# Performance work log

Measured on AMD Instinct MI355X. Metric: run time of the kernel, lower is better.

## Reference

```python
import jax, jax.numpy as jnp
import numpy as np
from jax import lax

# Module hyperparameters (from init_kwargs)
H, W, T = 80, 96, 112   # full-resolution feature volume size
C = 16                  # in_channel
K = 3                   # kernel_size (box filter)
D = 3                   # correlation window count per axis
SF = 2                  # correlation stride (sf)
CC = 2 * C + K ** 3     # conv1 in/out channels = 59


def _resize_axis_linear_ac(x, axis, out_size):
    """1D linear resize along `axis` with align_corners=True semantics."""
    in_size = x.shape[axis]
    pos = jnp.arange(out_size, dtype=x.dtype) * ((in_size - 1) / (out_size - 1))
    i0 = jnp.clip(jnp.floor(pos).astype(jnp.int32), 0, in_size - 2)
    w1 = pos - i0.astype(x.dtype)
    shp = [1] * x.ndim
    shp[axis] = out_size
    w1 = w1.reshape(shp)
    x0 = jnp.take(x, i0, axis=axis)
    x1 = jnp.take(x, i0 + 1, axis=axis)
    return x0 * (1.0 - w1) + x1 * w1


def upsample_trilinear_ac(x, factor=2):
    # matches nn.Upsample(scale_factor=2, mode='trilinear', align_corners=True)
    for axis in (2, 3, 4):
        x = _resize_axis_linear_ac(x, axis, x.shape[axis] * factor)
    return x


def _grid_sample_3d_one(src, coords):
    """src [C,H,W,T], coords [3,H,W,T] in voxel units.
    Trilinear sampling, zeros padding, align_corners=True (matches grid_sample)."""
    Hs, Ws, Ts = src.shape[1], src.shape[2], src.shape[3]
    cx, cy, cz = coords[0], coords[1], coords[2]
    x0 = jnp.floor(cx); y0 = jnp.floor(cy); z0 = jnp.floor(cz)
    fx = cx - x0; fy = cy - y0; fz = cz - z0
    x0i = x0.astype(jnp.int32); y0i = y0.astype(jnp.int32); z0i = z0.astype(jnp.int32)
    out = jnp.zeros_like(src)
    for dx in (0, 1):
        for dy in (0, 1):
            for dz in (0, 1):
                ix = x0i + dx; iy = y0i + dy; iz = z0i + dz
                valid = (ix >= 0) & (ix < Hs) & (iy >= 0) & (iy < Ws) & (iz >= 0) & (iz < Ts)
                v = src[:, jnp.clip(ix, 0, Hs - 1), jnp.clip(iy, 0, Ws - 1), jnp.clip(iz, 0, Ts - 1)]
                w = (fx if dx else 1.0 - fx) * (fy if dy else 1.0 - fy) * (fz if dz else 1.0 - fz)
                out = out + jnp.where(valid, w, 0.0)[None] * v
    return out


def spatial_transform(src, flow):
    # src [B,C,H,W,T], flow [B,3,H,W,T] (voxel displacement)
    grid = jnp.stack(jnp.meshgrid(jnp.arange(H), jnp.arange(W), jnp.arange(T), indexing='ij')).astype(src.dtype)
    coords = grid[None] + flow  # [B,3,H,W,T]
    return jax.vmap(_grid_sample_3d_one)(src, coords)


def _box3(x, pad):
    """Depthwise 3x3x3 ones-kernel conv with zero padding `pad` (separable box sum)."""
    x = jnp.pad(x, ((0, 0), (0, 0), (pad, pad), (pad, pad), (pad, pad)))
    for axis in (2, 3, 4):
        n = x.shape[axis]
        x = (lax.slice_in_dim(x, 0, n - 2, axis=axis)
             + lax.slice_in_dim(x, 1, n - 1, axis=axis)
             + lax.slice_in_dim(x, 2, n, axis=axis))
    return x


def correlation3d(mov, fix):
    Bh, Ch, Hh, Wh, Th = mov.shape
    pm = _box3(mov, 1)           # [B,C,H,W,T]
    pf = _box3(fix, SF + 1)      # [B,C,H+2*SF,W+2*SF,T+2*SF]
    vols = []
    for i in range(D):
        for j in range(D):
            for k in range(D):
                crop = pf[:, :, i * SF:i * SF + Hh, j * SF:j * SF + Wh, k * SF:k * SF + Th]
                vols.append(jnp.sum(pm * crop, axis=1))  # channel reduce -> [B,H,W,T]
    return jnp.stack(vols, axis=1) / float(K ** 3)        # [B,27,H,W,T]


def conv3d(x, w, b):
    y = lax.conv_general_dilated(x, w, window_strides=(1, 1, 1),
                                 padding=((1, 1), (1, 1), (1, 1)),
                                 dimension_numbers=('NCDHW', 'OIDHW', 'NCDHW'))
    return y + b[None, :, None, None, None]


def setup_inputs() -> dict:
    key = jax.random.key(0)
    ks = jax.random.split(key, 10)
    f32 = jnp.float32
    def n(k, shape, s=0.05):
        return jax.random.normal(k, shape, f32) * s
    return {
        'x': jax.random.normal(ks[0], (1, C, H, W, T), f32),
        'y': jax.random.normal(ks[1], (1, C, H, W, T), f32),
        'flow': jax.random.normal(ks[2], (1, 3, H // 2, W // 2, T // 2), f32),
        'w1a': n(ks[3], (CC, CC, 3, 3, 3)), 'b1a': jnp.zeros((CC,), f32),
        'w1b': n(ks[4], (C, CC, 3, 3, 3)), 'b1b': jnp.zeros((C,), f32),
        'w2a': n(ks[5], (C, C, 3, 3, 3)), 'b2a': jnp.zeros((C,), f32),
        'w2b': n(ks[6], (C, C, 3, 3, 3)), 'b2b': jnp.zeros((C,), f32),
        'wf': n(ks[7], (3, C, 3, 3, 3), 1e-5), 'bf': jnp.zeros((3,), f32),
    }


def reference(x, y, flow, w1a, b1a, w1b, b1b, w2a, b2a, w2b, b2b, wf, bf):
    # in_flow=True, scale=True: upsample 2*flow trilinearly, warp x
    flow_up = upsample_trilinear_ac(flow * 2.0)          # [B,3,H,W,T]
    xw = spatial_transform(x, flow_up)                   # warped moving features
    corr = correlation3d(xw, y)                          # [B,27,H,W,T]
    stack = jnp.concatenate([xw, corr, y], axis=1)       # [B,59,H,W,T]
    h = jax.nn.relu(conv3d(conv3d(stack, w1a, b1a), w1b, b1b))
    res = jax.nn.relu(conv3d(conv3d(h, w2a, b2a), w2b, b2b))
    return conv3d(h + res, wf, bf)                       # [B,3,H,W,T]
```

## Files before the change

kernel.cpp:

```cpp
#include <hip/hip_runtime.h>
#include <hip/hip_bf16.h>
#include <cstddef>
#include <type_traits>

typedef __hip_bfloat16 bf16;
typedef __attribute__((ext_vector_type(8))) short short8;
typedef __attribute__((ext_vector_type(4))) float f32x4;

constexpr int H = 80, W = 96, T = 112;
constexpr int N = H * W * T;
constexpr int WT = W * T;
constexpr int Hh = 40, Wh = 48, Th = 56;
constexpr int Nh = Hh * Wh * Th;
constexpr int PH = 84, PW = 100, PT = 116;
constexpr int NPF = PH * PW * PT;

static __device__ __forceinline__ float b2f(bf16 v) { return __bfloat162float(v); }
static __device__ __forceinline__ bf16  f2b(float v) { return __float2bfloat16(v); }
static __device__ __forceinline__ float us2f(unsigned short u) { return __uint_as_float(((unsigned)u) << 16); }

__global__ __launch_bounds__(256) void wbuild_kernel(const float* __restrict__ w, bf16* __restrict__ wb,
                                                     int COUT, int CIN, int KC_TOT, int NT_TOT)
{
    int idx = blockIdx.x * 256 + threadIdx.x;
    int total = 27 * KC_TOT * NT_TOT * 512;
    if (idx >= total) return;
    int j    = idx & 7;
    int lane = (idx >> 3) & 63;
    int rest = idx >> 9;
    int nt   = rest % NT_TOT; rest /= NT_TOT;
    int kc   = rest % KC_TOT;
    int tap  = rest / KC_TOT;
    int o    = nt * 16 + (lane & 15);
    int cin  = kc * 32 + (lane >> 4) * 8 + j;
    float val = (o < COUT && cin < CIN) ? w[((size_t)o * CIN + cin) * 27 + tap] : 0.f;
    wb[idx] = f2b(val);
}

__global__ __launch_bounds__(256) void bias_kernel(const float* __restrict__ b1a, const float* __restrict__ b1b,
                                                   const float* __restrict__ b2a, const float* __restrict__ b2b,
                                                   const float* __restrict__ bff, float* __restrict__ out)
{
    int i = threadIdx.x;
    if (i < 64)       out[i] = (i < 59) ? b1a[i] : 0.f;
    else if (i < 96)  { int j = i - 64;  out[i] = (j < 16) ? b1b[j] : 0.f; }
    else if (i < 128) { int j = i - 96;  out[i] = (j < 16) ? b2a[j] : 0.f; }
    else if (i < 160) { int j = i - 128; out[i] = (j < 16) ? b2b[j] : 0.f; }
    else if (i < 176) { int j = i - 160; out[i] = (j < 3)  ? bff[j] : 0.f; }
}

__global__ __launch_bounds__(256) void upsample_kernel(const float* __restrict__ flow,
                                                       float* __restrict__ flow_up)
{
    int idx = blockIdx.x * 256 + threadIdx.x;
    if (idx >= 3 * N) return;
    int c = idx / N, v = idx % N;
    int t = v % T; int hw = v / T; int w = hw % W; int h = hw / W;
    float ph = (float)h * ((float)(Hh - 1) / (float)(H - 1));
    float pw = (float)w * ((float)(Wh - 1) / (float)(W - 1));
    float pt = (float)t * ((float)(Th - 1) / (float)(T - 1));
    int i0 = min((int)ph, Hh - 2); float fh = ph - (float)i0;
    int j0 = min((int)pw, Wh - 2); float fw = pw - (float)j0;
    int k0 = min((int)pt, Th - 2); float ft = pt - (float)k0;
    const float* fp = flow + (size_t)c * Nh;
    auto L = [&](int a, int b, int d) -> float {
        return 2.0f * fp[((size_t)a * Wh + b) * Th + d];
    };
    float v000 = L(i0, j0, k0),     v001 = L(i0, j0, k0 + 1);
    float v010 = L(i0, j0 + 1, k0), v011 = L(i0, j0 + 1, k0 + 1);
    float v100 = L(i0 + 1, j0, k0),     v101 = L(i0 + 1, j0, k0 + 1);
    float v110 = L(i0 + 1, j0 + 1, k0), v111 = L(i0 + 1, j0 + 1, k0 + 1);
    float val = (1.f - fh) * ((1.f - fw) * ((1.f - ft) * v000 + ft * v001)
                            +        fw  * ((1.f - ft) * v010 + ft * v011))
              +        fh  * ((1.f - fw) * ((1.f - ft) * v100 + ft * v101)
                            +        fw  * ((1.f - ft) * v110 + ft * v111));
    flow_up[idx] = val;
}

__global__ __launch_bounds__(256) void warp_kernel(const float* __restrict__ x,
                                                   const float* __restrict__ flow_up,
                                                   bf16* __restrict__ xw)
{
    int v = blockIdx.x * 256 + threadIdx.x;
    if (v >= N) return;
    int t = v % T; int hw = v / T; int w = hw % W; int h = hw / W;
    float cx = (float)h + flow_up[v];
    float cy = (float)w + flow_up[N + v];
    float cz = (float)t + flow_up[2 * N + v];
    float fx0 = floorf(cx), fy0 = floorf(cy), fz0 = floorf(cz);
    float fx = cx - fx0, fy = cy - fy0, fz = cz - fz0;
    int ix = (int)fx0, iy = (int)fy0, iz = (int)fz0;

    float wc[8];
    int   oc[8];
    #pragma unroll
    for (int c8 = 0; c8 < 8; c8++) {
        int dx = (c8 >> 2) & 1, dy = (c8 >> 1) & 1, dz = c8 & 1;
        int ax = ix + dx, ay = iy + dy, az = iz + dz;
        bool ok = ((unsigned)ax < (unsigned)H) && ((unsigned)ay < (unsigned)W) && ((unsigned)az < (unsigned)T);
        float wt = (dx ? fx : 1.f - fx) * (dy ? fy : 1.f - fy) * (dz ? fz : 1.f - fz);
        wc[c8] = ok ? wt : 0.f;
        int cax = min(max(ax, 0), H - 1);
        int cay = min(max(ay, 0), W - 1);
        int caz = min(max(az, 0), T - 1);
        oc[c8] = (cax * W + cay) * T + caz;
    }
    #pragma unroll 1
    for (int c = 0; c < 16; c++) {
        const float* xp = x + (size_t)c * N;
        float s = 0.f;
        #pragma unroll
        for (int c8 = 0; c8 < 8; c8++) s += wc[c8] * xp[oc[c8]];
        xw[(size_t)c * N + v] = f2b(s);
    }
}

__global__ __launch_bounds__(256) void pm_kernel(const bf16* __restrict__ xw, bf16* __restrict__ pm)
{
    int idx = blockIdx.x * 256 + threadIdx.x;
    int ts = idx % 7;  int r = idx / 7;
    int w  = r % W;    r /= W;
    int h  = r % H;    int c = r / H;
    int t0 = ts * 16;

    float acc[16];
    #pragma unroll
    for (int k = 0; k < 16; k++) acc[k] = 0.f;

    const bf16* base = xw + (size_t)c * N;
    #pragma unroll
    for (int dh = -1; dh <= 1; dh++)
        #pragma unroll
        for (int dw = -1; dw <= 1; dw++) {
            int hh = h + dh, ww = w + dw;
            if (((unsigned)hh < (unsigned)H) && ((unsigned)ww < (unsigned)W)) {
                const unsigned short* rp = (const unsigned short*)(base + (size_t)(hh * W + ww) * T);
                float v[18];
                v[0] = (t0 > 0) ? us2f(rp[t0 - 1]) : 0.f;
                short8 cA = *(const short8*)(rp + t0);
                short8 cB = *(const short8*)(rp + t0 + 8);
                #pragma unroll
                for (int j = 0; j < 8; j++) v[1 + j] = us2f((unsigned short)cA[j]);
                #pragma unroll
                for (int j = 0; j < 8; j++) v[9 + j] = us2f((unsigned short)cB[j]);
                v[17] = (t0 + 16 < T) ? us2f(rp[t0 + 16]) : 0.f;
                #pragma unroll
                for (int k = 0; k < 16; k++) acc[k] += v[k] + v[k + 1] + v[k + 2];
            }
        }

    unsigned short ch[16];
    #pragma unroll
    for (int k = 0; k < 16; k++) { bf16 b = f2b(acc[k]); ch[k] = *(unsigned short*)&b; }
    uint4* dst = (uint4*)((unsigned short*)pm + (size_t)c * N + (size_t)(h * W + w) * T + t0);
    dst[0] = ((uint4*)ch)[0];
    dst[1] = ((uint4*)ch)[1];
}

__global__ __launch_bounds__(256) void pf_kernel(const float* __restrict__ y, bf16* __restrict__ pf)
{
    int idx = blockIdx.x * 256 + threadIdx.x;
    int ds = idx & 7;  int r = idx >> 3;
    int b  = r % PW;   r /= PW;
    int a  = r % PH;   int c = r / PH;
    int d0 = ds * 16;

    float acc[16];
    #pragma unroll
    for (int k = 0; k < 16; k++) acc[k] = 0.f;

    const float* base = y + (size_t)c * N;
    #pragma unroll
    for (int da = 0; da < 3; da++)
        #pragma unroll
        for (int db = 0; db < 3; db++) {
            int hh = a - 3 + da, ww = b - 3 + db;
            if (((unsigned)hh < (unsigned)H) && ((unsigned)ww < (unsigned)W)) {
                const float* rp = base + (size_t)(hh * W + ww) * T;
                float v[24];
                if (d0 >= 8) {
                    float4 a0 = *(const float4*)(rp + d0 - 8);
                    float4 a1 = *(const float4*)(rp + d0 - 4);
                    v[0] = a0.x; v[1] = a0.y; v[2] = a0.z; v[3] = a0.w;
                    v[4] = a1.x; v[5] = a1.y; v[6] = a1.z; v[7] = a1.w;
                } else {
                    #pragma unroll
                    for (int j = 0; j < 8; j++) v[j] = 0.f;
                }
                if (d0 <= 104) {
                    float4 b0 = *(const float4*)(rp + d0);
                    float4 b1 = *(const float4*)(rp + d0 + 4);
                    v[8]  = b0.x; v[9]  = b0.y; v[10] = b0.z; v[11] = b0.w;
                    v[12] = b1.x; v[13] = b1.y; v[14] = b1.z; v[15] = b1.w;
                } else {
                    #pragma unroll
                    for (int j = 8; j < 16; j++) v[j] = 0.f;
                }
                if (d0 <= 96) {
                    float4 c0 = *(const float4*)(rp + d0 + 8);
                    float4 c1 = *(const float4*)(rp + d0 + 12);
                    v[16] = c0.x; v[17] = c0.y; v[18] = c0.z; v[19] = c0.w;
                    v[20] = c1.x; v[21] = c1.y; v[22] = c1.z; v[23] = c1.w;
                } else {
                    #pragma unroll
                    for (int j = 16; j < 24; j++) v[j] = 0.f;
                }
                #pragma unroll
                for (int k = 0; k < 16; k++) acc[k] += v[k + 5] + v[k + 6] + v[k + 7];
            }
        }

    unsigned short ch[16];
    #pragma unroll
    for (int k = 0; k < 16; k++) { bf16 bb = f2b(acc[k]); ch[k] = *(unsigned short*)&bb; }
    uint2* dst = (uint2*)((unsigned short*)pf + (size_t)c * NPF + (size_t)(a * PW + b) * PT + d0);
    int nst = (d0 == 112) ? 1 : 4;
    #pragma unroll
    for (int k = 0; k < 4; k++) if (k < nst) dst[k] = ((uint2*)ch)[k];
}

__global__ __launch_bounds__(256) void corr_assemble_kernel(const bf16* __restrict__ pm,
                                                            const bf16* __restrict__ pf,
                                                            const bf16* __restrict__ xw,
                                                            const float* __restrict__ y,
                                                            bf16* __restrict__ stack)
{
    int v = blockIdx.x * 256 + threadIdx.x;
    if (v >= N) return;
    int t = v % T; int hw = v / T; int w = hw % W; int h = hw / W;

    float pmv[16];
    #pragma unroll
    for (int c = 0; c < 16; c++) pmv[c] = b2f(pm[(size_t)c * N + v]);

    float acc[27];
    #pragma unroll
    for (int i = 0; i < 27; i++) acc[i] = 0.f;

    const size_t pbase = ((size_t)h * PW + w) * PT + t;
    #pragma unroll 1
    for (int c = 0; c < 16; c++) {
        const bf16* pfc = pf + (size_t)c * NPF + pbase;
        float pv = pmv[c];
        #pragma unroll
        for (int i = 0; i < 3; i++)
            #pragma unroll
            for (int j = 0; j < 3; j++)
                #pragma unroll
                for (int k = 0; k < 3; k++)
                    acc[i * 9 + j * 3 + k] += pv * b2f(pfc[((size_t)(2 * i) * PW + 2 * j) * PT + 2 * k]);
    }

    unsigned short ch[64];
    #pragma unroll
    for (int c = 0; c < 16; c++) ch[c] = ((const unsigned short*)xw)[(size_t)c * N + v];
    #pragma unroll
    for (int i = 0; i < 27; i++) { bf16 b = f2b(acc[i] * (1.f / 27.f)); ch[16 + i] = *(unsigned short*)&b; }
    #pragma unroll
    for (int c = 0; c < 16; c++) { bf16 b = f2b(y[(size_t)c * N + v]); ch[43 + c] = *(unsigned short*)&b; }
    #pragma unroll
    for (int c = 59; c < 64; c++) ch[c] = 0;
    uint4* dst = (uint4*)((unsigned short*)stack + (size_t)v * 64);
    #pragma unroll
    for (int k = 0; k < 8; k++) dst[k] = ((uint4*)ch)[k];
}

__global__ __launch_bounds__(256) void corr_kernel(const bf16* __restrict__ pm, const bf16* __restrict__ pf,
                                                   bf16* __restrict__ corr_tmp)
{
    int v = blockIdx.x * 256 + threadIdx.x;
    if (v >= N) return;
    int t = v % T; int hw = v / T; int w = hw % W; int h = hw / W;
    float pmv[16];
    #pragma unroll
    for (int c = 0; c < 16; c++) pmv[c] = b2f(pm[(size_t)c * N + v]);
    #pragma unroll 1
    for (int i = 0; i < 3; i++)
    #pragma unroll 1
    for (int j = 0; j < 3; j++)
    #pragma unroll 1
    for (int k = 0; k < 3; k++) {
        size_t base = ((size_t)(2 * i + h) * PW + (2 * j + w)) * PT + (2 * k + t);
        float s = 0.f;
        #pragma unroll
        for (int c = 0; c < 16; c++) s += pmv[c] * b2f(pf[(size_t)c * NPF + base]);
        corr_tmp[(size_t)v * 28 + (i * 9 + j * 3 + k)] = f2b(s * (1.f / 27.f));
    }
}

__global__ __launch_bounds__(256) void assemble_kernel(const bf16* __restrict__ xw,
                                                       const bf16* __restrict__ corr_tmp,
                                                       const float* __restrict__ y,
                                                       bf16* __restrict__ stack)
{
    int v = blockIdx.x * 256 + threadIdx.x;
    if (v >= N) return;
    unsigned short ch[64];
    #pragma unroll
    for (int c = 0; c < 16; c++) ch[c] = ((const unsigned short*)xw)[(size_t)c * N + v];
    #pragma unroll
    for (int i = 0; i < 27; i++) ch[16 + i] = ((const unsigned short*)corr_tmp)[(size_t)v * 28 + i];
    #pragma unroll
    for (int c = 0; c < 16; c++) { bf16 b = f2b(y[(size_t)c * N + v]); ch[43 + c] = *(unsigned short*)&b; }
    #pragma unroll
    for (int c = 59; c < 64; c++) ch[c] = 0;
    uint4* dst = (uint4*)((unsigned short*)stack + (size_t)v * 64);
    #pragma unroll
    for (int k = 0; k < 8; k++) dst[k] = ((uint4*)ch)[k];
}

template <int CST_IN, int KC_TOT, int NT, int NT_TOT, int CST_OUT, bool RELU, int STORE>
__global__ __launch_bounds__(256, 3) void conv_lds(const bf16* __restrict__ in,
                                                   const bf16* __restrict__ wb,
                                                   const float* __restrict__ bias,
                                                   const bf16* __restrict__ aux,
                                                   void* __restrict__ out,
                                                   int kc_off, int nt_off)
{
    constexpr int KCP     = CST_IN / 32;
    constexpr int ASTRIDE = 80;
    constexpr int ZOFF    = 648 * ASTRIDE;
    __shared__ __align__(16) char smem[648 * ASTRIDE + 16];

    const int tid  = threadIdx.x;
    const int lane = tid & 63;
    const int n16  = lane & 15;
    const int q    = lane >> 4;
    const int wv   = tid >> 6;

    int bid = blockIdx.x;
    int cid = (bid & 7) * 420 + (bid >> 3);
    int t0  = (cid % 7) * 16;
    int rs  = cid / 7;
    int w0  = (rs % 24) * 4;
    int h0  = (rs / 24) * 4;
    const int h = h0 + wv;

    const bool interior = (h0 != 0) && (h0 != H - 4) && (w0 != 0) && (w0 != W - 4)
                       && (t0 != 0) && (t0 != T - 16);

    f32x4 acc[4][NT];
    #pragma unroll
    for (int nt = 0; nt < NT; ++nt) {
        float bv = (STORE == 1) ? 0.f : bias[nt * 16 + n16];
        #pragma unroll
        for (int m2 = 0; m2 < 4; ++m2)
            #pragma unroll
            for (int r = 0; r < 4; ++r) acc[m2][nt][r] = bv;
    }

    if (tid < 4) *(int*)(smem + ZOFF + tid * 4) = 0;

    const char* arow[4];
    #pragma unroll
    for (int m2 = 0; m2 < 4; ++m2)
        arow[m2] = smem + (size_t)(((wv * 6 + m2) * 18 + n16) * ASTRIDE) + q * 16;

    auto run = [&](auto chk_c) {
        constexpr bool CHK = decltype(chk_c)::value;
        unsigned msk[4];
        if (CHK) {
            #pragma unroll
            for (int m2 = 0; m2 < 4; ++m2) {
                int w = w0 + m2, t = t0 + n16;
                bool vh[3] = { h > 0, true, h < H - 1 };
                bool vw[3] = { w > 0, true, w < W - 1 };
                bool vt[3] = { t > 0, true, t < T - 1 };
                unsigned m = 0;
                #pragma unroll
                for (int tap = 0; tap < 27; ++tap)
                    if (vh[tap / 9] && vw[(tap % 9) / 3] && vt[tap % 3]) m |= (1u << tap);
                msk[m2] = m;
            }
        }

        #pragma unroll 1
        for (int kcp = 0; kcp < KCP; ++kcp) {
            if (kcp > 0) __syncthreads();
            #pragma unroll 1
            for (int it = 0; it < 11; ++it) {
                int slot = it * 64 + (tid >> 2);
                if (slot < 648) {
                    int hh = slot / 108, rm = slot - hh * 108;
                    int ww = rm / 18,    tt = rm - ww * 18;
                    int gh = min(max(h0 - 1 + hh, 0), H - 1);
                    int gw = min(max(w0 - 1 + ww, 0), W - 1);
                    int gt = min(max(t0 - 1 + tt, 0), T - 1);
                    const char* gp = (const char*)in + (size_t)((gh * W + gw) * T + gt) * (CST_IN * 2)
                                     + kcp * 64 + (tid & 3) * 16;
                    *(uint4*)(smem + slot * ASTRIDE + (tid & 3) * 16) = *(const uint4*)gp;
                }
            }
            __syncthreads();

            const size_t TAPB = (size_t)KC_TOT * NT_TOT * 1024;
            const char* wbt = (const char*)wb
                            + ((size_t)(kcp + kc_off) * NT_TOT + nt_off) * 1024
                            + (size_t)lane * 16;
            int rowoff = 0, c3 = 0, tshift = 0;

            #pragma unroll 1
            for (int g = 0; g < 9; ++g) {
                short8 bv[3][NT];
                #pragma unroll
                for (int dt = 0; dt < 3; ++dt)
                    #pragma unroll
                    for (int nt = 0; nt < NT; ++nt)
                        bv[dt][nt] = *(const short8*)(wbt + dt * TAPB + nt * 1024);

                short8 av[3][4];
                #pragma unroll
                for (int m2 = 0; m2 < 4; ++m2) {
                    const char* p = arow[m2] + rowoff;
                    #pragma unroll
                    for (int dt = 0; dt < 3; ++dt) {
                        const char* q2;
                        if (CHK) {
                            bool ok = (msk[m2] >> (tshift + dt)) & 1u;
                            q2 = ok ? (p + dt * ASTRIDE) : (smem + ZOFF);
                        } else {
                            q2 = p + dt * ASTRIDE;
                        }
                        av[dt][m2] = *(const short8*)q2;
                    }
                }

                #pragma unroll
                for (int dt = 0; dt < 3; ++dt)
                    #pragma unroll
                    for (int nt = 0; nt < NT; ++nt)
                        #pragma unroll
                        for (int m2 = 0; m2 < 4; ++m2)
                            acc[m2][nt] = __builtin_amdgcn_mfma_f32_16x16x32_bf16(av[dt][m2], bv[dt][nt], acc[m2][nt], 0, 0, 0);

                wbt += 3 * TAPB;
                tshift += 3;
                if (c3 == 2) { rowoff += 4 * 1440; c3 = 0; }
                else         { rowoff += 1440;     c3++;   }
            }
        }
    };
    if (interior) run(std::integral_constant<bool, false>{});
    else          run(std::integral_constant<bool, true>{});

    #pragma unroll
    for (int m2 = 0; m2 < 4; ++m2) {
        int vrow = (h * W + (w0 + m2)) * T + t0 + q * 4;
        #pragma unroll
        for (int r = 0; r < 4; ++r) {
            int v = vrow + r;
            #pragma unroll
            for (int nt = 0; nt < NT; ++nt) {
                float x = acc[m2][nt][r];
                if (STORE == 2 && nt == 0) x += b2f(aux[(size_t)v * 16 + n16]);
                if (RELU && STORE != 4) x = fmaxf(x, 0.f);
                if (STORE == 4) x = fmaxf(x, 0.f) + b2f(aux[(size_t)v * CST_OUT + nt * 16 + n16]);
                if (STORE == 1) {
                    if (nt == 0) ((bf16*)out)[(size_t)v * 16 + n16] = f2b(x);
                } else if (STORE == 3) {
                    int ch = nt * 16 + n16;
                    if (ch < 3) ((float*)out)[(size_t)ch * N + v] = x;
                } else {
                    ((bf16*)out)[(size_t)v * CST_OUT + nt * 16 + n16] = f2b(x);
                }
            }
        }
    }
}

extern "C" void kernel_launch(void* const* d_in, const int* in_sizes, int n_in,
                              void* d_out, int out_size, void* d_ws, size_t ws_size,
                              hipStream_t stream)
{
    (void)in_sizes; (void)n_in; (void)out_size;
    const float* x_p   = (const float*)d_in[0];
    const float* y_p   = (const float*)d_in[1];
    const float* flow_p= (const float*)d_in[2];
    const float* w1a_p = (const float*)d_in[3];
    const float* b1a_p = (const float*)d_in[4];
    const float* w1b_p = (const float*)d_in[5];
    const float* b1b_p = (const float*)d_in[6];
    const float* w2a_p = (const float*)d_in[7];
    const float* b2a_p = (const float*)d_in[8];
    const float* w2b_p = (const float*)d_in[9];
    const float* b2b_p = (const float*)d_in[10];
    const float* wf_p  = (const float*)d_in[11];
    const float* bf_p  = (const float*)d_in[12];

    char* wsb = (char*)d_ws;
    const size_t NB32 = (size_t)N * 32 * 2;
    const size_t NB64 = 2 * NB32;
    const size_t WSUM = (110592 + 55296 + 27648 + 27648 + 13824);
    const size_t NEED_BIG = 2 * NB64 + WSUM * 2 + 176 * 4 + 256;
    const bool BIG = (ws_size >= NEED_BIG);

    bf16 *stack, *buf1, *pm, *pf, *xw, *corr_tmp, *hbuf, *t2buf, *sumbuf, *hpart, *buf1h;
    float* flow_up; bf16* wroot;
    if (BIG) {
        stack    = (bf16*)wsb;
        flow_up  = (float*)wsb;
        hbuf     = (bf16*)wsb;
        t2buf    = (bf16*)(wsb + NB32);
        buf1     = (bf16*)(wsb + NB64);
        xw       = (bf16*)(wsb + NB64);
        pm       = (bf16*)(wsb + NB64 + (size_t)16 * N * 2);
        pf       = (bf16*)(wsb + NB64 + (size_t)32 * N * 2);
        sumbuf   = (bf16*)(wsb + NB64);
        corr_tmp = nullptr; hpart = nullptr; buf1h = nullptr;
        wroot    = (bf16*)(wsb + 2 * NB64);
    } else {
        const size_t A_off = 0, B_off = 2 * NB32, C_off = 3 * NB32;
        const size_t D_off = C_off + (size_t)N * 16 * 2;
        pf       = (bf16*)(wsb + A_off);
        pm       = (bf16*)(wsb + A_off + (size_t)16 * NPF * 2);
        flow_up  = (float*)(wsb + A_off + (size_t)16 * NPF * 2 + (size_t)16 * N * 2);
        stack    = (bf16*)(wsb + A_off);
        hbuf     = (bf16*)(wsb + A_off);
        t2buf    = (bf16*)(wsb + A_off + NB32);
        corr_tmp = (bf16*)(wsb + B_off);
        buf1h    = (bf16*)(wsb + B_off);
        sumbuf   = (bf16*)(wsb + B_off);
        xw       = (bf16*)(wsb + C_off);
        hpart    = (bf16*)(wsb + C_off);
        buf1     = nullptr;
        wroot    = (bf16*)(wsb + D_off);
    }
    bf16*  wb1a  = wroot;
    bf16*  wb1b  = wb1a + 110592;
    bf16*  wb2a  = wb1b + 55296;
    bf16*  wb2b  = wb2a + 27648;
    bf16*  wbf   = wb2b + 27648;
    float* biasp = (float*)(wbf + 13824);

    wbuild_kernel<<<432, 256, 0, stream>>>(w1a_p, wb1a, 59, 59, 2, 4);
    wbuild_kernel<<<216, 256, 0, stream>>>(w1b_p, wb1b, 16, 59, 2, 2);
    wbuild_kernel<<<108, 256, 0, stream>>>(w2a_p, wb2a, 16, 16, 1, 2);
    wbuild_kernel<<<108, 256, 0, stream>>>(w2b_p, wb2b, 16, 16, 1, 2);
    wbuild_kernel<<<54,  256, 0, stream>>>(wf_p,  wbf,  3,  16, 1, 1);
    bias_kernel<<<1, 256, 0, stream>>>(b1a_p, b1b_p, b2a_p, b2b_p, bf_p, biasp);

    upsample_kernel<<<3 * N / 256, 256, 0, stream>>>(flow_p, flow_up);
    warp_kernel<<<N / 256, 256, 0, stream>>>(x_p, flow_up, xw);
    pm_kernel<<<N / 256, 256, 0, stream>>>(xw, pm);
    pf_kernel<<<16 * PH * PW * 8 / 256, 256, 0, stream>>>(y_p, pf);
    if (BIG) {
        corr_assemble_kernel<<<N / 256, 256, 0, stream>>>(pm, pf, xw, y_p, stack);
    } else {
        corr_kernel<<<N / 256, 256, 0, stream>>>(pm, pf, corr_tmp);
        assemble_kernel<<<N / 256, 256, 0, stream>>>(xw, corr_tmp, y_p, stack);
    }

    const int GB = N / 256;
    if (BIG) {
        conv_lds<64, 2, 4, 4, 64, false, 0><<<GB, 256, 0, stream>>>(stack, wb1a, biasp + 0,   nullptr, buf1,  0, 0);
        conv_lds<64, 2, 2, 2, 32, true,  0><<<GB, 256, 0, stream>>>(buf1,  wb1b, biasp + 64,  nullptr, hbuf,  0, 0);
    } else {
        conv_lds<64, 2, 2, 4, 32, false, 0><<<GB, 256, 0, stream>>>(stack, wb1a, biasp + 0,   nullptr, buf1h, 0, 0);
        conv_lds<32, 2, 2, 2, 32, false, 1><<<GB, 256, 0, stream>>>(buf1h, wb1b, biasp,       nullptr, hpart, 0, 0);
        conv_lds<64, 2, 2, 4, 32, false, 0><<<GB, 256, 0, stream>>>(stack, wb1a, biasp + 32,  nullptr, buf1h, 0, 2);
        conv_lds<32, 2, 2, 2, 32, true,  2><<<GB, 256, 0, stream>>>(buf1h, wb1b, biasp + 64,  hpart,   hbuf,  1, 0);
    }
    conv_lds<32, 1, 2, 2, 32, false, 0><<<GB, 256, 0, stream>>>(hbuf,  wb2a, biasp + 96,  nullptr, t2buf,  0, 0);
    conv_lds<32, 1, 2, 2, 32, false, 4><<<GB, 256, 0, stream>>>(t2buf, wb2b, biasp + 128, hbuf,    sumbuf, 0, 0);
    conv_lds<32, 1, 1, 1, 16, false, 3><<<GB, 256, 0, stream>>>(sumbuf, wbf, biasp + 160, nullptr, d_out,  0, 0);
}
```

Measured before the change: 979.6 us.

## Double-buffer weight fragment loads and hoist halo-load index math in conv kernel

The global weight fragments for each tap group are now prefetched into a second register buffer while the MFMAs for the current group run, so global-load latency overlaps with compute. The halo tile fill replaces an 11-iteration loop with per-slot divisions by a 6-iteration unrolled loop that reuses w/t offsets computed once per thread. A-operand LDS reads are interleaved per dt with their MFMAs. The cost is higher register pressure from the two B buffers, which may lower occupancy or cause spills.

```diff
diff --git a/kernel.cpp b/kernel.cpp
--- a/kernel.cpp
+++ b/kernel.cpp
@@ -351,6 +351,16 @@
 
     if (tid < 4) *(int*)(smem + ZOFF + tid * 4) = 0;
 
+    const int sA = tid >> 2, pA = tid & 3;
+    const int wwA = sA / 18, ttA = sA - wwA * 18;
+    const int gvA = (min(max(w0 - 1 + wwA, 0), W - 1)) * T + min(max(t0 - 1 + ttA, 0), T - 1);
+    const int ldA = sA * ASTRIDE + pA * 16;
+    const int sB = 64 + sA;
+    const bool hasB = tid < 176;
+    const int wwB = sB / 18, ttB = sB - wwB * 18;
+    const int gvB = (min(max(w0 - 1 + wwB, 0), W - 1)) * T + min(max(t0 - 1 + ttB, 0), T - 1);
+    const int ldB = sB * ASTRIDE + pA * 16;
+
     const char* arow[4];
     #pragma unroll
     for (int m2 = 0; m2 < 4; ++m2)
@@ -377,67 +387,72 @@
         #pragma unroll 1
         for (int kcp = 0; kcp < KCP; ++kcp) {
             if (kcp > 0) __syncthreads();
-            #pragma unroll 1
-            for (int it = 0; it < 11; ++it) {
-                int slot = it * 64 + (tid >> 2);
-                if (slot < 648) {
-                    int hh = slot / 108, rm = slot - hh * 108;
-                    int ww = rm / 18,    tt = rm - ww * 18;
-                    int gh = min(max(h0 - 1 + hh, 0), H - 1);
-                    int gw = min(max(w0 - 1 + ww, 0), W - 1);
-                    int gt = min(max(t0 - 1 + tt, 0), T - 1);
-                    const char* gp = (const char*)in + (size_t)((gh * W + gw) * T + gt) * (CST_IN * 2)
-                                     + kcp * 64 + (tid & 3) * 16;
-                    *(uint4*)(smem + slot * ASTRIDE + (tid & 3) * 16) = *(const uint4*)gp;
-                }
+            const char* inb = (const char*)in + kcp * 64 + pA * 16;
+            #pragma unroll
+            for (int hh = 0; hh < 6; ++hh) {
+                int gh  = min(max(h0 - 1 + hh, 0), H - 1);
+                int ghw = gh * WT;
+                *(uint4*)(smem + hh * (108 * ASTRIDE) + ldA) =
+                    *(const uint4*)(inb + (size_t)(ghw + gvA) * (CST_IN * 2));
+                if (hasB)
+                    *(uint4*)(smem + hh * (108 * ASTRIDE) + ldB) =
+                        *(const uint4*)(inb + (size_t)(ghw + gvB) * (CST_IN * 2));
             }
             __syncthreads();
 
             const size_t TAPB = (size_t)KC_TOT * NT_TOT * 1024;
-            const char* wbt = (const char*)wb
+            const char* wbn = (const char*)wb
                             + ((size_t)(kcp + kc_off) * NT_TOT + nt_off) * 1024
                             + (size_t)lane * 16;
-            int rowoff = 0, c3 = 0, tshift = 0;
-
-            #pragma unroll 1
-            for (int g = 0; g < 9; ++g) {
-                short8 bv[3][NT];
+
+            short8 bvA[3][NT], bvB[3][NT];
+            auto loadB = [&](short8 (&bv)[3][NT]) {
                 #pragma unroll
                 for (int dt = 0; dt < 3; ++dt)
                     #pragma unroll
                     for (int nt = 0; nt < NT; ++nt)
-                        bv[dt][nt] = *(const short8*)(wbt + dt * TAPB + nt * 1024);
-
-                short8 av[3][4];
-                #pragma unroll
-                for (int m2 = 0; m2 < 4; ++m2) {
-                    const char* p = arow[m2] + rowoff;
+                        bv[dt][nt] = *(const short8*)(wbn + dt * TAPB + nt * 1024);
+                wbn += 3 * TAPB;
+            };
+
+            int rowoff = 0, c3 = 0, tsh = 0;
+            auto advance = [&]() {
+                if (c3 == 2) { rowoff += 4 * 1440; c3 = 0; }
+                else         { rowoff += 1440;     c3++;   }
+                tsh += 3;
+            };
+            auto computeG = [&](short8 (&bv)[3][NT]) {
+                #pragma unroll
+                for (int dt = 0; dt < 3; ++dt) {
+                    short8 av[4];
                     #pragma unroll
-                    for (int dt = 0; dt < 3; ++dt) {
-                        const char* q2;
+                    for (int m2 = 0; m2 < 4; ++m2) {
+                        const char* p;
                         if (CHK) {
-                            bool ok = (msk[m2] >> (tshift + dt)) & 1u;
-                            q2 = ok ? (p + dt * ASTRIDE) : (smem + ZOFF);
+                            bool ok = (msk[m2] >> (tsh + dt)) & 1u;
+                            p = ok ? (arow[m2] + rowoff + dt * ASTRIDE) : (smem + ZOFF);
                         } else {
-                            q2 = p + dt * ASTRIDE;
+                            p = arow[m2] + rowoff + dt * ASTRIDE;
                         }
-                        av[dt][m2] = *(const short8*)q2;
+                        av[m2] = *(const short8*)p;
                     }
-                }
-
-                #pragma unroll
-                for (int dt = 0; dt < 3; ++dt)
                     #pragma unroll
                     for (int nt = 0; nt < NT; ++nt)
                         #pragma unroll
                         for (int m2 = 0; m2 < 4; ++m2)
-                            acc[m2][nt] = __builtin_amdgcn_mfma_f32_16x16x32_bf16(av[dt][m2], bv[dt][nt], acc[m2][nt], 0, 0, 0);
-
-                wbt += 3 * TAPB;
-                tshift += 3;
-                if (c3 == 2) { rowoff += 4 * 1440; c3 = 0; }
-                else         { rowoff += 1440;     c3++;   }
+                            acc[m2][nt] = __builtin_amdgcn_mfma_f32_16x16x32_bf16(av[m2], bv[dt][nt], acc[m2][nt], 0, 0, 0);
+                }
+            };
+
+            loadB(bvA);
+            #pragma unroll 1
+            for (int gp = 0; gp < 4; ++gp) {
+                loadB(bvB);
+                computeG(bvA); advance();
+                loadB(bvA);
+                computeG(bvB); advance();
             }
+            computeG(bvA);
         }
     };
     if (interior) run(std::integral_constant<bool, false>{});
```

New measurement: 1.002 ms. 2.3% more time.
